# Kernel optimization log

Measured on AMD Instinct MI355X. Metric: run time of the kernel, lower is better.

The kernel has to match this reference:

```python
import jax, jax.numpy as jnp
import numpy as np

N_NODES = 131072       # 64 graphs * 2048 nodes
N_EDGES = 2097152      # avg degree 16
N_GRAPHS = 64
NODES_PER_GRAPH = 2048
D_IN = 128
D_EMB = 64
D_HID = 128
N_ACT = 2048


def setup_inputs() -> dict:
    key = jax.random.key(0)
    ks = jax.random.split(key, 12)
    s = lambda d: 1.0 / np.sqrt(d)
    return {
        "x": jax.random.normal(ks[0], (N_NODES, D_IN), dtype=jnp.float32),
        "edge_index": jax.random.randint(ks[1], (2, N_EDGES), 0, N_NODES, dtype=jnp.int32),
        "W1l": jax.random.normal(ks[2], (D_EMB, D_IN), dtype=jnp.float32) * s(D_IN),
        "b1l": jnp.zeros((D_EMB,), dtype=jnp.float32),
        "W1r": jax.random.normal(ks[3], (D_EMB, D_IN), dtype=jnp.float32) * s(D_IN),
        "W2l": jax.random.normal(ks[4], (D_EMB, D_EMB), dtype=jnp.float32) * s(D_EMB),
        "b2l": jnp.zeros((D_EMB,), dtype=jnp.float32),
        "W2r": jax.random.normal(ks[5], (D_EMB, D_EMB), dtype=jnp.float32) * s(D_EMB),
        "fc1_W": jax.random.normal(ks[6], (D_HID, D_EMB), dtype=jnp.float32) * s(D_EMB),
        "fc1_b": jnp.zeros((D_HID,), dtype=jnp.float32),
        "fc2_W": jax.random.normal(ks[7], (N_ACT, D_HID), dtype=jnp.float32) * s(D_HID),
        "fc2_b": jnp.zeros((N_ACT,), dtype=jnp.float32),
    }


def _sage_conv(x, src, dst, Wl, bl, Wr):
    # PyG SAGEConv (mean aggr): out = lin_l(mean_{j in N(i)} x_j) + lin_r(x_i)
    msg = x[src]                                              # [E, D] gather
    agg = jax.ops.segment_sum(msg, dst, num_segments=N_NODES)  # [N, D]
    cnt = jax.ops.segment_sum(jnp.ones((src.shape[0],), x.dtype), dst,
                              num_segments=N_NODES)
    mean = agg / jnp.maximum(cnt, 1.0)[:, None]
    return mean @ Wl.T + bl + x @ Wr.T


def reference(x, edge_index, W1l, b1l, W1r, W2l, b2l, W2r,
              fc1_W, fc1_b, fc2_W, fc2_b):
    src, dst = edge_index[0], edge_index[1]
    h1 = _sage_conv(x, src, dst, W1l, b1l, W1r)    # [N, D_EMB]
    h2 = _sage_conv(h1, src, dst, W2l, b2l, W2r)   # [N, D_EMB]
    g = h2.reshape(N_GRAPHS, NODES_PER_GRAPH, D_EMB).mean(axis=1)  # [B, D_EMB]
    h = jax.nn.relu(g @ fc1_W.T + fc1_b)
    q_values = h @ fc2_W.T + fc2_b                 # [B, N_ACT]
    return q_values
```

## Files before the change

### kernel.cpp

```cpp
#include <hip/hip_runtime.h>
#include <hip/hip_bf16.h>

#define D_IN 128
#define D_EMB 64

typedef float f32x2 __attribute__((ext_vector_type(2)));
typedef float f32x4v __attribute__((ext_vector_type(4)));
typedef short bf16x8 __attribute__((ext_vector_type(8)));

static __device__ __forceinline__ unsigned short f2bf(float f) {
  __hip_bfloat16 h = __float2bfloat16(f);
  return *(unsigned short*)&h;
}
static __device__ __forceinline__ float bf2f(unsigned short u) {
  return __uint_as_float((unsigned)u << 16);
}

__global__ __launch_bounds__(256) void wprep_mfma_k(const float* __restrict__ W,
                                                    unsigned short* __restrict__ out,
                                                    int K) {
  int tid = blockIdx.x * 256 + threadIdx.x;
  int total = (K / 32) * 4 * 64;
  if (tid >= total) return;
  int lane = tid & 63;
  int ct = (tid >> 6) & 3;
  int s = tid >> 8;
  int row = ct * 16 + (lane & 15);
  int kk = s * 32 + (lane >> 4) * 8;
  unsigned short tmp[8];
#pragma unroll
  for (int j = 0; j < 8; j++) tmp[j] = f2bf(W[row * K + kk + j]);
  *(uint4*)&out[(size_t)tid * 8] = *(uint4*)tmp;
}


__global__ __launch_bounds__(256) void bhist1_k(const int* __restrict__ key,
                                                int* __restrict__ bh, int E) {
  __shared__ int h[256];
  const int t = threadIdx.x;
  h[t] = 0;
  __syncthreads();
  const int base = blockIdx.x * 2048;
#pragma unroll
  for (int j = 0; j < 8; j++) {
    int e = base + j * 256 + t;
    if (e < E) atomicAdd(&h[key[e] >> 9], 1);
  }
  __syncthreads();
  bh[t * 1024 + blockIdx.x] = h[t];
}

__global__ __launch_bounds__(256) void scanA_k(int* __restrict__ bh,
                                               int* __restrict__ bintot) {
  __shared__ int sa[256], sb[256];
  const int t = threadIdx.x;
  int* row = bh + (size_t)blockIdx.x * 1024;
  int v0 = row[t * 4], v1 = row[t * 4 + 1], v2 = row[t * 4 + 2], v3 = row[t * 4 + 3];
  int sum = v0 + v1 + v2 + v3;
  sa[t] = sum;
  __syncthreads();
  int* in = sa;
  int* out = sb;
  for (int st = 1; st < 256; st <<= 1) {
    out[t] = in[t] + (t >= st ? in[t - st] : 0);
    __syncthreads();
    int* tmp = in; in = out; out = tmp;
  }
  int excl = in[t] - sum;
  row[t * 4] = excl;
  row[t * 4 + 1] = excl + v0;
  row[t * 4 + 2] = excl + v0 + v1;
  row[t * 4 + 3] = excl + v0 + v1 + v2;
  if (t == 255) bintot[blockIdx.x] = in[255];
}

__global__ __launch_bounds__(256) void scanB_k(const int* __restrict__ bintot,
                                               int* __restrict__ base) {
  __shared__ int sa[256], sb[256];
  const int t = threadIdx.x;
  int v = bintot[t];
  sa[t] = v;
  __syncthreads();
  int* in = sa;
  int* out = sb;
  for (int st = 1; st < 256; st <<= 1) {
    out[t] = in[t] + (t >= st ? in[t - st] : 0);
    __syncthreads();
    int* tmp = in; in = out; out = tmp;
  }
  base[t] = in[t] - v;
  if (t == 255) base[256] = in[255];
}

__global__ __launch_bounds__(256) void sfill_k(const int* __restrict__ src,
                                               const int* __restrict__ dst,
                                               const int* __restrict__ sh,
                                               const int* __restrict__ ssub,
                                               int* __restrict__ srcS,
                                               int* __restrict__ dstS, int E) {
  __shared__ int hA[256], hB[256], runCur[256], gb[256];
  __shared__ int scache[2048];
  __shared__ int dcache[2048];
  __shared__ int sortS[2048];
  __shared__ int sortD[2048];
  __shared__ unsigned short subb[2048];
  const int t = threadIdx.x;
  const int base = blockIdx.x * 2048;
  const int n = min(2048, E - base);
  hA[t] = 0;
  __syncthreads();
#pragma unroll
  for (int j = 0; j < 8; j++) {
    int idx = j * 256 + t;
    int e = base + idx;
    if (idx < n) {
      int s = src[e];
      scache[idx] = s;
      dcache[idx] = dst[e];
      atomicAdd(&hA[s >> 9], 1);
    }
  }
  __syncthreads();
  int cnt = hA[t];
  int* in = hA;
  int* out = hB;
  for (int st = 1; st < 256; st <<= 1) {
    out[t] = in[t] + (t >= st ? in[t - st] : 0);
    __syncthreads();
    int* tmp = in; in = out; out = tmp;
  }
  int rs = in[t] - cnt;
  __syncthreads();
  hB[t] = rs;
  runCur[t] = rs;
  gb[t] = ssub[t] + sh[t * 1024 + blockIdx.x];
  __syncthreads();
#pragma unroll
  for (int j = 0; j < 8; j++) {
    int idx = j * 256 + t;
    if (idx < n) {
      int s = scache[idx];
      int b = s >> 9;
      int lpos = atomicAdd(&runCur[b], 1);
      sortS[lpos] = s;
      sortD[lpos] = dcache[idx];
      subb[lpos] = (unsigned short)b;
    }
  }
  __syncthreads();
  for (int idx = t; idx < n; idx += 256) {
    int b = subb[idx];
    int g = gb[b] + idx - hB[b];
    srcS[g] = sortS[idx];
    dstS[g] = sortD[idx];
  }
}

__global__ __launch_bounds__(256) void bfill1_k(const int* __restrict__ src,
                                                const int* __restrict__ dst,
                                                const int* __restrict__ bh,
                                                const int* __restrict__ sbase,
                                                unsigned int* __restrict__ bkt,
                                                int E) {
  __shared__ int hA[256], hB[256], runCur[256], gb[256];
  __shared__ int dcache[2048];
  __shared__ unsigned int sorted[2048];
  __shared__ unsigned short subb[2048];
  const int t = threadIdx.x;
  const int base = blockIdx.x * 2048;
  const int n = min(2048, E - base);
  hA[t] = 0;
  __syncthreads();
#pragma unroll
  for (int j = 0; j < 8; j++) {
    int idx = j * 256 + t;
    int e = base + idx;
    if (idx < n) {
      int d = dst[e];
      dcache[idx] = d;
      atomicAdd(&hA[d >> 9], 1);
    }
  }
  __syncthreads();
  int cnt = hA[t];
  int* in = hA;
  int* out = hB;
  for (int st = 1; st < 256; st <<= 1) {
    out[t] = in[t] + (t >= st ? in[t - st] : 0);
    __syncthreads();
    int* tmp = in; in = out; out = tmp;
  }
  int rs = in[t] - cnt;
  __syncthreads();
  hB[t] = rs;
  runCur[t] = rs;
  gb[t] = sbase[t] + bh[t * 1024 + blockIdx.x];
  __syncthreads();
#pragma unroll
  for (int j = 0; j < 8; j++) {
    int idx = j * 256 + t;
    int e = base + idx;
    if (idx < n) {
      int d = dcache[idx];
      int b = d >> 9;
      int lpos = atomicAdd(&runCur[b], 1);
      sorted[lpos] = ((unsigned)(d & 511) << 17) | (unsigned)src[e];
      subb[lpos] = (unsigned short)b;
    }
  }
  __syncthreads();
  for (int idx = t; idx < n; idx += 256) {
    int b = subb[idx];
    bkt[gb[b] + idx - hB[b]] = sorted[idx];
  }
}

__global__ __launch_bounds__(256) void deg4_k(const unsigned int* __restrict__ bkt,
                                              const int* __restrict__ sbase,
                                              int* __restrict__ deg) {
  __shared__ int h[512];
  const int t = threadIdx.x;
  h[t] = 0;
  h[t + 256] = 0;
  __syncthreads();
  const int i = blockIdx.x;
  const int lo = sbase[i], hi = sbase[i + 1];
  for (int e = lo + t; e < hi; e += 256) atomicAdd(&h[bkt[e] >> 17], 1);
  __syncthreads();
  deg[i * 512 + t] = h[t];
  deg[i * 512 + t + 256] = h[t + 256];
}

__global__ __launch_bounds__(256) void blocksum_k(const int* __restrict__ deg,
                                                  int* __restrict__ bsum) {
  __shared__ int sm[256];
  int t = threadIdx.x;
  sm[t] = deg[blockIdx.x * 256 + t];
  __syncthreads();
  for (int s = 128; s > 0; s >>= 1) {
    if (t < s) sm[t] += sm[t + s];
    __syncthreads();
  }
  if (t == 0) bsum[blockIdx.x] = sm[0];
}

__global__ __launch_bounds__(256) void scanbsum_k(int* __restrict__ bsum) {
  __shared__ int a[512], b[512];
  int t = threadIdx.x;
  a[t] = bsum[t];
  a[t + 256] = bsum[t + 256];
  __syncthreads();
  int* in = a;
  int* out = b;
  for (int st = 1; st < 512; st <<= 1) {
    for (int i = t; i < 512; i += 256) out[i] = in[i] + (i >= st ? in[i - st] : 0);
    __syncthreads();
    int* tmp = in; in = out; out = tmp;
  }
  for (int i = t; i < 512; i += 256) bsum[i] = (i == 0) ? 0 : in[i - 1];
}

__global__ __launch_bounds__(256) void rowptr_k(const int* __restrict__ deg,
                                                const int* __restrict__ bsumEx,
                                                int* __restrict__ rowPtr,
                                                float* __restrict__ invdeg) {
  __shared__ int a[256], b[256];
  int t = threadIdx.x;
  int i = blockIdx.x * 256 + t;
  int d = deg[i];
  a[t] = d;
  __syncthreads();
  int* in = a;
  int* out = b;
  for (int st = 1; st < 256; st <<= 1) {
    out[t] = in[t] + (t >= st ? in[t - st] : 0);
    __syncthreads();
    int* tmp = in; in = out; out = tmp;
  }
  int incl = in[t] + bsumEx[blockIdx.x];
  rowPtr[i + 1] = incl;
  invdeg[i] = 1.0f / fmaxf((float)d, 1.0f);
  if (i == 0) rowPtr[0] = 0;
}

#define CSR_CAP 12032
__global__ __launch_bounds__(256) void scat4_k(const unsigned int* __restrict__ bkt,
                                               const int* __restrict__ sbase,
                                               const int* __restrict__ rowPtr,
                                               int* __restrict__ csr) {
  __shared__ int cur[512];
  __shared__ int cbuf[CSR_CAP];
  const int t = threadIdx.x;
  const int i = blockIdx.x;
  const int node0 = i * 512;
  const int base0 = rowPtr[node0];
  cur[t] = rowPtr[node0 + t] - base0;
  cur[t + 256] = rowPtr[node0 + t + 256] - base0;
  __syncthreads();
  const int lo = sbase[i], hi = sbase[i + 1];
  for (int e = lo + t; e < hi; e += 256) {
    unsigned v = bkt[e];
    int pos = atomicAdd(&cur[v >> 17], 1);
    int sval = (int)(v & 0x1FFFFu);
    if (pos < CSR_CAP) cbuf[pos] = sval;
    else csr[base0 + pos] = sval;
  }
  __syncthreads();
  const int cnt = rowPtr[node0 + 512] - base0;
  const int lim = cnt < CSR_CAP ? cnt : CSR_CAP;
  for (int idx = t; idx < lim; idx += 256) csr[base0 + idx] = cbuf[idx];
}

__global__ __launch_bounds__(256) void nperm_k(const int* __restrict__ deg,
                                               int* __restrict__ perm) {
  __shared__ int dg[256];
  const int t = threadIdx.x;
  const int n0 = blockIdx.x * 256;
  int myd = deg[n0 + t];
  dg[t] = myd;
  __syncthreads();
  const int g0 = t & ~63;
  int rank = 0;
#pragma unroll
  for (int j = 0; j < 64; j++) {
    int dj = dg[g0 + j];
    rank += (dj < myd) || (dj == myd && (g0 + j) < t);
  }
  perm[n0 + g0 + rank] = n0 + t;
}

__global__ __launch_bounds__(256) void gemm1_k(const float4* __restrict__ x4,
                                               const unsigned short* __restrict__ wb1,
                                               const unsigned short* __restrict__ wb2,
                                               const float* __restrict__ bias2,
                                               unsigned char* __restrict__ out1,
                                               unsigned short* __restrict__ out2) {
  constexpr int K = 128, K4 = K / 4;
  const int t = threadIdx.x;
  const int lane = t & 63;
  const int wv = t >> 6;
  const int col = lane & 15;
  const int quad = lane >> 4;
  const int nb = blockIdx.x * 64;
  const int arow = nb + wv * 16 + col;
  f32x4v acc1[4], acc2[4];
#pragma unroll
  for (int ct = 0; ct < 4; ct++) {
    acc1[ct] = (f32x4v){0.f, 0.f, 0.f, 0.f};
    float bj = bias2[ct * 16 + col];
    acc2[ct] = (f32x4v){bj, bj, bj, bj};
  }
#pragma unroll
  for (int s = 0; s < K / 32; s++) {
    float4 f0 = x4[(size_t)arow * K4 + s * 8 + quad * 2];
    float4 f1 = x4[(size_t)arow * K4 + s * 8 + quad * 2 + 1];
    unsigned short h[8];
    h[0] = f2bf(f0.x); h[1] = f2bf(f0.y); h[2] = f2bf(f0.z); h[3] = f2bf(f0.w);
    h[4] = f2bf(f1.x); h[5] = f2bf(f1.y); h[6] = f2bf(f1.z); h[7] = f2bf(f1.w);
    bf16x8 a = *(const bf16x8*)h;
#pragma unroll
    for (int ct = 0; ct < 4; ct++) {
      bf16x8 b1 = *(const bf16x8*)&wb1[(size_t)((s * 4 + ct) * 64 + lane) * 8];
      acc1[ct] = __builtin_amdgcn_mfma_f32_16x16x32_bf16(a, b1, acc1[ct], 0, 0, 0);
      bf16x8 b2 = *(const bf16x8*)&wb2[(size_t)((s * 4 + ct) * 64 + lane) * 8];
      acc2[ct] = __builtin_amdgcn_mfma_f32_16x16x32_bf16(a, b2, acc2[ct], 0, 0, 0);
    }
  }
#pragma unroll
  for (int ct = 0; ct < 4; ct++) {
#pragma unroll
    for (int reg = 0; reg < 4; reg++) {
      int node = nb + wv * 16 + quad * 4 + reg;
      unsigned pk = (unsigned)__builtin_amdgcn_cvt_pk_fp8_f32(acc1[ct][reg],
                                                              acc1[ct][reg], 0, false);
      out1[(size_t)node * 64 + ct * 16 + col] = (unsigned char)(pk & 0xff);
      out2[(size_t)node * 64 + ct * 16 + col] = f2bf(acc2[ct][reg]);
    }
  }
}

#define LROW 72
__global__ __launch_bounds__(256) void gatherf_k(const uint4* __restrict__ yb,
                                                 const int* __restrict__ csr,
                                                 const int* __restrict__ rowPtr,
                                                 const float* __restrict__ invdeg,
                                                 const unsigned short* __restrict__ xr,
                                                 const int* __restrict__ perm,
                                                 const unsigned short* __restrict__ wb2,
                                                 unsigned char* __restrict__ y2,
                                                 float* __restrict__ pm) {
  __shared__ float sg[4][4][16];
  __shared__ unsigned short sh1[64 * LROW];
  __shared__ int sp[64];
  const int t = threadIdx.x;
  if (t < 64) sp[t] = perm[blockIdx.x * 64 + t];
  __syncthreads();
  const int lane = t & 63;
  const int wv = t >> 6;
  const int q = lane & 3;
  const int nl = lane >> 2;
  const int n = sp[wv * 16 + nl];
  const int rp0 = rowPtr[n], rp1 = rowPtr[n + 1];
  float acc[16];
#pragma unroll
  for (int k = 0; k < 16; k++) acc[k] = 0.f;
  for (int e = rp0; e < rp1; e++) {
    int s = csr[e];
    uint4 v = yb[(size_t)s * 4 + q];
    f32x2 p;
    p = __builtin_amdgcn_cvt_pk_f32_fp8(v.x, false); acc[0] += p.x;  acc[1] += p.y;
    p = __builtin_amdgcn_cvt_pk_f32_fp8(v.x, true);  acc[2] += p.x;  acc[3] += p.y;
    p = __builtin_amdgcn_cvt_pk_f32_fp8(v.y, false); acc[4] += p.x;  acc[5] += p.y;
    p = __builtin_amdgcn_cvt_pk_f32_fp8(v.y, true);  acc[6] += p.x;  acc[7] += p.y;
    p = __builtin_amdgcn_cvt_pk_f32_fp8(v.z, false); acc[8] += p.x;  acc[9] += p.y;
    p = __builtin_amdgcn_cvt_pk_f32_fp8(v.z, true);  acc[10] += p.x; acc[11] += p.y;
    p = __builtin_amdgcn_cvt_pk_f32_fp8(v.w, false); acc[12] += p.x; acc[13] += p.y;
    p = __builtin_amdgcn_cvt_pk_f32_fp8(v.w, true);  acc[14] += p.x; acc[15] += p.y;
  }
  const float sc = invdeg[n];
  float gacc[16];
  {
    const int nloc = wv * 16 + nl;
    unsigned short hh[16];
#pragma unroll
    for (int u = 0; u < 4; u++) {
      ushort4 ob = *(const ushort4*)&xr[(size_t)n * 64 + q * 16 + u * 4];
      float v0 = acc[4 * u + 0] * sc + bf2f(ob.x);
      float v1 = acc[4 * u + 1] * sc + bf2f(ob.y);
      float v2 = acc[4 * u + 2] * sc + bf2f(ob.z);
      float v3 = acc[4 * u + 3] * sc + bf2f(ob.w);
      gacc[4 * u + 0] = v0; gacc[4 * u + 1] = v1;
      gacc[4 * u + 2] = v2; gacc[4 * u + 3] = v3;
      hh[4 * u + 0] = f2bf(v0); hh[4 * u + 1] = f2bf(v1);
      hh[4 * u + 2] = f2bf(v2); hh[4 * u + 3] = f2bf(v3);
    }
    *(uint4*)&sh1[nloc * LROW + q * 16] = *(uint4*)&hh[0];
    *(uint4*)&sh1[nloc * LROW + q * 16 + 8] = *(uint4*)&hh[8];
  }
#pragma unroll
  for (int m = 4; m <= 32; m <<= 1)
#pragma unroll
    for (int k = 0; k < 16; k++) gacc[k] += __shfl_xor(gacc[k], m, 64);
  if (nl == 0) {
#pragma unroll
    for (int k = 0; k < 16; k++) sg[wv][q][k] = gacc[k];
  }
  __syncthreads();
  if (t < 64) {
    int qq = t >> 4, k = t & 15;
    float tot = sg[0][qq][k] + sg[1][qq][k] + sg[2][qq][k] + sg[3][qq][k];
    pm[((size_t)(blockIdx.x >> 5) * 32 + (blockIdx.x & 31)) * 64 + t] = tot;
  }
  {
    const int col = lane & 15;
    const int quad = lane >> 4;
    f32x4v a2[4];
#pragma unroll
    for (int ct = 0; ct < 4; ct++) a2[ct] = (f32x4v){0.f, 0.f, 0.f, 0.f};
#pragma unroll
    for (int s = 0; s < 2; s++) {
      bf16x8 a = *(const bf16x8*)&sh1[(wv * 16 + col) * LROW + s * 32 + quad * 8];
#pragma unroll
      for (int ct = 0; ct < 4; ct++) {
        bf16x8 b = *(const bf16x8*)&wb2[(size_t)((s * 4 + ct) * 64 + lane) * 8];
        a2[ct] = __builtin_amdgcn_mfma_f32_16x16x32_bf16(a, b, a2[ct], 0, 0, 0);
      }
    }
#pragma unroll
    for (int ct = 0; ct < 4; ct++) {
#pragma unroll
      for (int reg = 0; reg < 4; reg++) {
        int node = sp[wv * 16 + quad * 4 + reg];
        unsigned pk = (unsigned)__builtin_amdgcn_cvt_pk_fp8_f32(a2[ct][reg],
                                                                a2[ct][reg], 0, false);
        y2[(size_t)node * 64 + ct * 16 + col] = (unsigned char)(pk & 0xff);
      }
    }
  }
}

__global__ __launch_bounds__(256) void gatherp_k(const uint4* __restrict__ yb,
                                                 const int* __restrict__ csr,
                                                 const int* __restrict__ rowPtr,
                                                 const float* __restrict__ invdeg,
                                                 const int* __restrict__ perm,
                                                 float* __restrict__ pm) {
  __shared__ float sg[4][4][16];
  __shared__ int sp[64];
  const int t = threadIdx.x;
  if (t < 64) sp[t] = perm[blockIdx.x * 64 + t];
  __syncthreads();
  const int lane = t & 63;
  const int wv = t >> 6;
  const int q = lane & 3;
  const int nl = lane >> 2;
  const int n = sp[wv * 16 + nl];
  const int rp0 = rowPtr[n], rp1 = rowPtr[n + 1];
  float acc[16];
#pragma unroll
  for (int k = 0; k < 16; k++) acc[k] = 0.f;
  for (int e = rp0; e < rp1; e++) {
    int s = csr[e];
    uint4 v = yb[(size_t)s * 4 + q];
    f32x2 p;
    p = __builtin_amdgcn_cvt_pk_f32_fp8(v.x, false); acc[0] += p.x;  acc[1] += p.y;
    p = __builtin_amdgcn_cvt_pk_f32_fp8(v.x, true);  acc[2] += p.x;  acc[3] += p.y;
    p = __builtin_amdgcn_cvt_pk_f32_fp8(v.y, false); acc[4] += p.x;  acc[5] += p.y;
    p = __builtin_amdgcn_cvt_pk_f32_fp8(v.y, true);  acc[6] += p.x;  acc[7] += p.y;
    p = __builtin_amdgcn_cvt_pk_f32_fp8(v.z, false); acc[8] += p.x;  acc[9] += p.y;
    p = __builtin_amdgcn_cvt_pk_f32_fp8(v.z, true);  acc[10] += p.x; acc[11] += p.y;
    p = __builtin_amdgcn_cvt_pk_f32_fp8(v.w, false); acc[12] += p.x; acc[13] += p.y;
    p = __builtin_amdgcn_cvt_pk_f32_fp8(v.w, true);  acc[14] += p.x; acc[15] += p.y;
  }
  const float sc = invdeg[n];
  float gacc[16];
#pragma unroll
  for (int k = 0; k < 16; k++) gacc[k] = acc[k] * sc;
#pragma unroll
  for (int m = 4; m <= 32; m <<= 1)
#pragma unroll
    for (int k = 0; k < 16; k++) gacc[k] += __shfl_xor(gacc[k], m, 64);
  if (nl == 0) {
#pragma unroll
    for (int k = 0; k < 16; k++) sg[wv][q][k] = gacc[k];
  }
  __syncthreads();
  if (t < 64) {
    int qq = t >> 4, k = t & 15;
    float tot = sg[0][qq][k] + sg[1][qq][k] + sg[2][qq][k] + sg[3][qq][k];
    pm[((size_t)(blockIdx.x >> 5) * 32 + (blockIdx.x & 31)) * 64 + t] = tot;
  }
}

__global__ __launch_bounds__(256) void reduce_both_k(const float* __restrict__ p1,
                                                     const float* __restrict__ p2,
                                                     float* __restrict__ gm1,
                                                     float* __restrict__ gm2) {
  int half = blockIdx.x >> 4;
  int idx = (blockIdx.x & 15) * 256 + threadIdx.x;
  const float* pm = half ? p2 : p1;
  float* gm = half ? gm2 : gm1;
  int b = idx >> 6, j = idx & 63;
  float acc = 0.0f;
  for (int blk = 0; blk < 32; blk++) acc += pm[((size_t)b * 32 + blk) * 64 + j];
  gm[idx] = acc * (1.0f / 2048.0f);
}

__global__ __launch_bounds__(256) void combine_k(const float* __restrict__ gmean2,
                                                 const float* __restrict__ gmean1,
                                                 const float* __restrict__ b2l,
                                                 const float* __restrict__ W2r,
                                                 float* __restrict__ g) {
  int idx = blockIdx.x * 256 + threadIdx.x;
  int b = idx >> 6, j = idx & 63;
  const float4* m4 = (const float4*)(gmean1 + b * 64);
  const float4* w4 = (const float4*)(W2r + j * 64);
  float acc = gmean2[idx] + b2l[j];
#pragma unroll
  for (int k4 = 0; k4 < 16; k4++) {
    float4 mv = m4[k4], wv = w4[k4];
    acc += mv.x * wv.x + mv.y * wv.y + mv.z * wv.z + mv.w * wv.w;
  }
  g[idx] = acc;
}

__global__ __launch_bounds__(256) void mlp1_k(const float* __restrict__ g,
                                              const float* __restrict__ fc1_W,
                                              const float* __restrict__ fc1_b,
                                              float* __restrict__ h) {
  int idx = blockIdx.x * 256 + threadIdx.x;
  int b = idx >> 7, k = idx & 127;
  const float4* g4 = (const float4*)(g + b * 64);
  const float4* w4 = (const float4*)(fc1_W + k * 64);
  float acc = fc1_b[k];
#pragma unroll
  for (int j4 = 0; j4 < 16; j4++) {
    float4 gv = g4[j4], wv = w4[j4];
    acc += gv.x * wv.x + gv.y * wv.y + gv.z * wv.z + gv.w * wv.w;
  }
  h[idx] = fmaxf(acc, 0.0f);
}

__global__ __launch_bounds__(256) void mlp2_k(const float* __restrict__ h,
                                              const float* __restrict__ fc2_W,
                                              const float* __restrict__ fc2_b,
                                              float* __restrict__ out) {
  __shared__ float4 sh[32];
  int b = blockIdx.x >> 3;
  int a = (blockIdx.x & 7) * 256 + threadIdx.x;
  if (threadIdx.x < 32) sh[threadIdx.x] = ((const float4*)(h + b * 128))[threadIdx.x];
  __syncthreads();
  const float4* w4 = (const float4*)(fc2_W + (size_t)a * 128);
  float acc = fc2_b[a];
#pragma unroll
  for (int k4 = 0; k4 < 32; k4++) {
    float4 hv = sh[k4], wv = w4[k4];
    acc += hv.x * wv.x + hv.y * wv.y + hv.z * wv.z + hv.w * wv.w;
  }
  out[b * 2048 + a] = acc;
}

extern "C" void kernel_launch(void* const* d_in, const int* in_sizes, int n_in,
                              void* d_out, int out_size, void* d_ws, size_t ws_size,
                              hipStream_t stream) {
  const float* x     = (const float*)d_in[0];
  const int*   ei    = (const int*)d_in[1];
  const float* W1l   = (const float*)d_in[2];
  const float* b1l   = (const float*)d_in[3];
  const float* W1r   = (const float*)d_in[4];
  const float* W2l   = (const float*)d_in[5];
  const float* b2l   = (const float*)d_in[6];
  const float* W2r   = (const float*)d_in[7];
  const float* fc1_W = (const float*)d_in[8];
  const float* fc1_b = (const float*)d_in[9];
  const float* fc2_W = (const float*)d_in[10];
  const float* fc2_b = (const float*)d_in[11];
  float* out = (float*)d_out;

  const int N = in_sizes[0] / D_IN;
  const int E = in_sizes[1] / 2;
  const int* src = ei;
  const int* dst = ei + E;

  char* ws = (char*)d_ws;
  int*   deg    = (int*)ws;     ws += (size_t)N * 4;
  int*   rowPtr = (int*)ws;     ws += (size_t)(N + 256) * 4;
  int*   bsum   = (int*)ws;     ws += 512 * 4;
  float* invdeg = (float*)ws;   ws += (size_t)N * 4;
  int*   perm   = (int*)ws;     ws += (size_t)N * 4;
  float* gmean1 = (float*)ws;   ws += 4096 * 4;
  float* gmean2 = (float*)ws;   ws += 4096 * 4;
  float* g      = (float*)ws;   ws += 4096 * 4;
  float* hbuf   = (float*)ws;   ws += 8192 * 4;
  unsigned short* wb1l = (unsigned short*)ws;  ws += 8192 * 2;
  unsigned short* wb1r = (unsigned short*)ws;  ws += 8192 * 2;
  unsigned short* wb2l = (unsigned short*)ws;  ws += 4096 * 2;
  int*   sh     = (int*)ws;     ws += (size_t)256 * 1024 * 4;
  int*   bh     = (int*)ws;     ws += (size_t)256 * 1024 * 4;
  int*   tot    = (int*)ws;     ws += 256 * 4;
  int*   ssub   = (int*)ws;     ws += 260 * 4;
  int*   sbase  = (int*)ws;     ws += 260 * 4;
  float* p1     = (float*)ws;   ws += (size_t)64 * 32 * 64 * 4;
  float* p2     = (float*)ws;   ws += (size_t)64 * 32 * 64 * 4;
  unsigned int* bkt = (unsigned int*)ws;  ws += (size_t)E * 4;
  int*   csr    = (int*)ws;     ws += (size_t)E * 4;
  unsigned char* bufA = (unsigned char*)ws;  ws += (size_t)64 * N;
  unsigned char* bufD = (unsigned char*)ws;  ws += (size_t)64 * N;
  unsigned short* bufB = (unsigned short*)ws;  ws += (size_t)64 * N * 2;
  size_t used = (size_t)(ws - (char*)d_ws);

  int* srcS = (int*)bufD;
  int* dstS = (int*)bufA;

  hipMemsetAsync(d_ws, 0, used, stream);

  wprep_mfma_k<<<4, 256, 0, stream>>>(W1l, wb1l, 128);
  wprep_mfma_k<<<4, 256, 0, stream>>>(W1r, wb1r, 128);
  wprep_mfma_k<<<2, 256, 0, stream>>>(W2l, wb2l, 64);

  const int nch = (E + 2047) >> 11;
  bhist1_k<<<nch, 256, 0, stream>>>(src, sh, E);
  scanA_k<<<256, 256, 0, stream>>>(sh, tot);
  scanB_k<<<1, 256, 0, stream>>>(tot, ssub);
  sfill_k<<<nch, 256, 0, stream>>>(src, dst, sh, ssub, srcS, dstS, E);
  bhist1_k<<<nch, 256, 0, stream>>>(dstS, bh, E);
  scanA_k<<<256, 256, 0, stream>>>(bh, tot);
  scanB_k<<<1, 256, 0, stream>>>(tot, sbase);
  bfill1_k<<<nch, 256, 0, stream>>>(srcS, dstS, bh, sbase, bkt, E);
  deg4_k<<<256, 256, 0, stream>>>(bkt, sbase, deg);
  blocksum_k<<<N / 256, 256, 0, stream>>>(deg, bsum);
  scanbsum_k<<<1, 256, 0, stream>>>(bsum);
  rowptr_k<<<N / 256, 256, 0, stream>>>(deg, bsum, rowPtr, invdeg);
  scat4_k<<<256, 256, 0, stream>>>(bkt, sbase, rowPtr, csr);
  nperm_k<<<N / 256, 256, 0, stream>>>(deg, perm);

  gemm1_k<<<N / 64, 256, 0, stream>>>((const float4*)x, wb1l, wb1r, b1l, bufA, bufB);
  gatherf_k<<<N / 64, 256, 0, stream>>>((const uint4*)bufA, csr, rowPtr, invdeg,
                                        bufB, perm, wb2l, bufD, p1);
  gatherp_k<<<N / 64, 256, 0, stream>>>((const uint4*)bufD, csr, rowPtr, invdeg,
                                        perm, p2);
  reduce_both_k<<<32, 256, 0, stream>>>(p1, p2, gmean1, gmean2);

  combine_k<<<16, 256, 0, stream>>>(gmean2, gmean1, b2l, W2r, g);
  mlp1_k<<<32, 256, 0, stream>>>(g, fc1_W, fc1_b, hbuf);
  mlp2_k<<<512, 256, 0, stream>>>(hbuf, fc2_W, fc2_b, out);
}
```

Measured before the change: 346.1 us.

## Drop source pre-sort pass and sort CSR neighbor lists locally in shared memory

Removes the first radix pass that presorted edges by source (histogram, scan, sfill kernels), bucketing edges directly by destination instead. To keep neighbor lists ordered by source within each row, which presumably matters for gather locality and deterministic summation order, each node's CSR segment is now insertion-sorted in shared memory inside the scatter kernel. It also merges the three weight-prep launches into one. This saves several full passes over the edge arrays, at the cost of per-row serial insertion sorts of about 16 elements, and segments that overflow the shared cache stay unsorted.

```diff
diff --git a/kernel.cpp b/kernel.cpp
--- a/kernel.cpp
+++ b/kernel.cpp
@@ -16,10 +16,19 @@
   return __uint_as_float((unsigned)u << 16);
 }
 
-__global__ __launch_bounds__(256) void wprep_mfma_k(const float* __restrict__ W,
-                                                    unsigned short* __restrict__ out,
-                                                    int K) {
-  int tid = blockIdx.x * 256 + threadIdx.x;
+__global__ __launch_bounds__(256) void wprep_all_k(const float* __restrict__ W1l,
+                                                   const float* __restrict__ W1r,
+                                                   const float* __restrict__ W2l,
+                                                   unsigned short* __restrict__ o1,
+                                                   unsigned short* __restrict__ o2,
+                                                   unsigned short* __restrict__ o3) {
+  const int b = blockIdx.x;
+  const float* W;
+  unsigned short* out;
+  int K, tid;
+  if (b < 4)      { W = W1l; out = o1; K = 128; tid = b * 256 + threadIdx.x; }
+  else if (b < 8) { W = W1r; out = o2; K = 128; tid = (b - 4) * 256 + threadIdx.x; }
+  else            { W = W2l; out = o3; K = 64;  tid = (b - 8) * 256 + threadIdx.x; }
   int total = (K / 32) * 4 * 64;
   if (tid >= total) return;
   int lane = tid & 63;
@@ -90,70 +99,6 @@
   }
   base[t] = in[t] - v;
   if (t == 255) base[256] = in[255];
-}
-
-__global__ __launch_bounds__(256) void sfill_k(const int* __restrict__ src,
-                                               const int* __restrict__ dst,
-                                               const int* __restrict__ sh,
-                                               const int* __restrict__ ssub,
-                                               int* __restrict__ srcS,
-                                               int* __restrict__ dstS, int E) {
-  __shared__ int hA[256], hB[256], runCur[256], gb[256];
-  __shared__ int scache[2048];
-  __shared__ int dcache[2048];
-  __shared__ int sortS[2048];
-  __shared__ int sortD[2048];
-  __shared__ unsigned short subb[2048];
-  const int t = threadIdx.x;
-  const int base = blockIdx.x * 2048;
-  const int n = min(2048, E - base);
-  hA[t] = 0;
-  __syncthreads();
-#pragma unroll
-  for (int j = 0; j < 8; j++) {
-    int idx = j * 256 + t;
-    int e = base + idx;
-    if (idx < n) {
-      int s = src[e];
-      scache[idx] = s;
-      dcache[idx] = dst[e];
-      atomicAdd(&hA[s >> 9], 1);
-    }
-  }
-  __syncthreads();
-  int cnt = hA[t];
-  int* in = hA;
-  int* out = hB;
-  for (int st = 1; st < 256; st <<= 1) {
-    out[t] = in[t] + (t >= st ? in[t - st] : 0);
-    __syncthreads();
-    int* tmp = in; in = out; out = tmp;
-  }
-  int rs = in[t] - cnt;
-  __syncthreads();
-  hB[t] = rs;
-  runCur[t] = rs;
-  gb[t] = ssub[t] + sh[t * 1024 + blockIdx.x];
-  __syncthreads();
-#pragma unroll
-  for (int j = 0; j < 8; j++) {
-    int idx = j * 256 + t;
-    if (idx < n) {
-      int s = scache[idx];
-      int b = s >> 9;
-      int lpos = atomicAdd(&runCur[b], 1);
-      sortS[lpos] = s;
-      sortD[lpos] = dcache[idx];
-      subb[lpos] = (unsigned short)b;
-    }
-  }
-  __syncthreads();
-  for (int idx = t; idx < n; idx += 256) {
-    int b = subb[idx];
-    int g = gb[b] + idx - hB[b];
-    srcS[g] = sortS[idx];
-    dstS[g] = sortD[idx];
-  }
 }
 
 __global__ __launch_bounds__(256) void bfill1_k(const int* __restrict__ src,
@@ -304,6 +249,18 @@
     int sval = (int)(v & 0x1FFFFu);
     if (pos < CSR_CAP) cbuf[pos] = sval;
     else csr[base0 + pos] = sval;
+  }
+  __syncthreads();
+  for (int nn = t; nn < 512; nn += 256) {
+    int s0 = rowPtr[node0 + nn] - base0;
+    int s1 = rowPtr[node0 + nn + 1] - base0;
+    if (s1 > CSR_CAP) s1 = CSR_CAP;
+    for (int a = s0 + 1; a < s1; a++) {
+      int key = cbuf[a];
+      int j = a - 1;
+      while (j >= s0 && cbuf[j] > key) { cbuf[j + 1] = cbuf[j]; j--; }
+      cbuf[j + 1] = key;
+    }
   }
   __syncthreads();
   const int cnt = rowPtr[node0 + 512] - base0;
@@ -635,10 +592,8 @@
   unsigned short* wb1l = (unsigned short*)ws;  ws += 8192 * 2;
   unsigned short* wb1r = (unsigned short*)ws;  ws += 8192 * 2;
   unsigned short* wb2l = (unsigned short*)ws;  ws += 4096 * 2;
-  int*   sh     = (int*)ws;     ws += (size_t)256 * 1024 * 4;
   int*   bh     = (int*)ws;     ws += (size_t)256 * 1024 * 4;
   int*   tot    = (int*)ws;     ws += 256 * 4;
-  int*   ssub   = (int*)ws;     ws += 260 * 4;
   int*   sbase  = (int*)ws;     ws += 260 * 4;
   float* p1     = (float*)ws;   ws += (size_t)64 * 32 * 64 * 4;
   float* p2     = (float*)ws;   ws += (size_t)64 * 32 * 64 * 4;
@@ -649,24 +604,15 @@
   unsigned short* bufB = (unsigned short*)ws;  ws += (size_t)64 * N * 2;
   size_t used = (size_t)(ws - (char*)d_ws);
 
-  int* srcS = (int*)bufD;
-  int* dstS = (int*)bufA;
-
   hipMemsetAsync(d_ws, 0, used, stream);
 
-  wprep_mfma_k<<<4, 256, 0, stream>>>(W1l, wb1l, 128);
-  wprep_mfma_k<<<4, 256, 0, stream>>>(W1r, wb1r, 128);
-  wprep_mfma_k<<<2, 256, 0, stream>>>(W2l, wb2l, 64);
+  wprep_all_k<<<10, 256, 0, stream>>>(W1l, W1r, W2l, wb1l, wb1r, wb2l);
 
   const int nch = (E + 2047) >> 11;
-  bhist1_k<<<nch, 256, 0, stream>>>(src, sh, E);
-  scanA_k<<<256, 256, 0, stream>>>(sh, tot);
-  scanB_k<<<1, 256, 0, stream>>>(tot, ssub);
-  sfill_k<<<nch, 256, 0, stream>>>(src, dst, sh, ssub, srcS, dstS, E);
-  bhist1_k<<<nch, 256, 0, stream>>>(dstS, bh, E);
+  bhist1_k<<<nch, 256, 0, stream>>>(dst, bh, E);
   scanA_k<<<256, 256, 0, stream>>>(bh, tot);
   scanB_k<<<1, 256, 0, stream>>>(tot, sbase);
-  bfill1_k<<<nch, 256, 0, stream>>>(srcS, dstS, bh, sbase, bkt, E);
+  bfill1_k<<<nch, 256, 0, stream>>>(src, dst, bh, sbase, bkt, E);
   deg4_k<<<256, 256, 0, stream>>>(bkt, sbase, deg);
   blocksum_k<<<N / 256, 256, 0, stream>>>(deg, bsum);
   scanbsum_k<<<1, 256, 0, stream>>>(bsum);
```

Measured after the change: 375.1 us. 8.4% more time.
